# Optimization experiments

Hardware: AMD Instinct MI355X
Metric: run time of the kernel (lower is better)

## Reference

```python
import jax, jax.numpy as jnp
import numpy as np

# Model dims (match init_kwargs / input_specs)
B, L, D = 4, 1024, 512
CHI, S = 32, 4          # bond_dim, spatial_bond_dim
TRUNC_THR = 1e-4        # relative SVD truncation threshold
LN_EPS = 1e-6


def setup_inputs() -> dict:
    key = jax.random.key(0)
    ks = jax.random.split(key, 6)
    def dense(k, fi, fo):
        return jax.random.normal(k, (fi, fo), jnp.float32) / np.float32(np.sqrt(fi))
    return {
        "x": jax.random.normal(ks[0], (B, L, D), jnp.float32),
        "W_site": dense(ks[1], D, CHI * S * CHI),
        "b_site": jnp.zeros((CHI * S * CHI,), jnp.float32),
        "W_bridge": dense(ks[2], S * CHI, CHI),
        "b_bridge": jnp.zeros((CHI,), jnp.float32),
        "W_out": dense(ks[3], CHI, D),
        "b_out": jnp.zeros((D,), jnp.float32),
        "gamma": jnp.ones((D,), jnp.float32),
        "beta": jnp.zeros((D,), jnp.float32),
        "W_gate": dense(ks[4], D, D),
        "b_gate": jnp.zeros((D,), jnp.float32),
    }


def _mps_temporal_scan(x, site_weights):
    """Sequential O(L*chi^2) MPS scan with per-step SVD truncation.

    x: [B, L, D]; site_weights: [B, L, chi, s, chi].
    State h_t [B, chi] is the (normalized) left environment vector. Each step
    contracts the left vector (state + input injection from the first chi
    features, since initial_state is zeros) with the site tensor, truncates
    small singular values (relative threshold), and accumulates log-norms.
    Returns outputs [B, L, s*chi] and log_probs [B, L].
    """
    u_seq = jnp.transpose(x[:, :, :CHI], (1, 0, 2))            # [L, B, chi]
    A_seq = jnp.transpose(site_weights, (1, 0, 2, 3, 4))        # [L, B, chi, s, chi]

    def step(h, inp):
        A, u = inp                                              # [B,chi,s,chi], [B,chi]
        left = h + u                                            # input-driven left vector
        M = jnp.einsum('bl,blpr->bpr', left, A)                 # [B, s, chi]
        U, Sv, Vh = jnp.linalg.svd(M, full_matrices=False)      # Sv: [B, min(s,chi)]
        mask = (Sv >= TRUNC_THR * Sv[:, :1]).astype(M.dtype)    # relative truncation
        St = Sv * mask
        Mt = jnp.einsum('bik,bk,bkr->bir', U, St, Vh)           # truncated site matrix
        nrm = jnp.sqrt(jnp.sum(St * St, axis=-1) + 1e-12)       # Frobenius norm -> log prob
        v = jnp.sum(Mt, axis=1)                                 # contract physical index
        h_new = v / (jnp.linalg.norm(v, axis=-1, keepdims=True) + 1e-12)
        return h_new, (Mt.reshape(Mt.shape[0], -1), jnp.log(nrm))

    h0 = jnp.zeros((x.shape[0], CHI), x.dtype)                  # initial_state = zeros
    _, (outs, logp) = jax.lax.scan(step, h0, (A_seq, u_seq))
    return jnp.transpose(outs, (1, 0, 2)), jnp.transpose(logp, (1, 0))


def reference(x, W_site, b_site, W_bridge, b_bridge, W_out, b_out,
              gamma, beta, W_gate, b_gate):
    x = x.astype(jnp.float32)
    Bb, Ll = x.shape[0], x.shape[1]
    # site_tensor_proj: Dense(chi*s*chi) applied directly to inputs
    site_weights = (x @ W_site + b_site).reshape(Bb, Ll, CHI, S, CHI)
    outs, _logp = _mps_temporal_scan(x, site_weights)           # [B, L, s*chi]
    y = outs @ W_bridge + b_bridge                              # mps_bridge -> [B,L,chi]
    y = y @ W_out + b_out                                       # output_projection -> [B,L,D]
    # LayerNorm(eps=1e-6)
    mu = jnp.mean(y, axis=-1, keepdims=True)
    var = jnp.mean((y - mu) ** 2, axis=-1, keepdims=True)
    yn = (y - mu) * jax.lax.rsqrt(var + LN_EPS) * gamma + beta
    # gated residual
    gate = jax.nn.sigmoid(x @ W_gate + b_gate)
    return gate * yn + (1.0 - gate) * x
```

## Files before the change

kernel.cpp:

```cpp
#include <hip/hip_runtime.h>
#include <math.h>

#define B_   4
#define L_   1024
#define D_   512
#define CHI_ 32
#define S_   4
#define BT_  (B_ * L_)
#define NC_  2560
#define DPRE 8

__device__ __forceinline__ float readlane_f(float v, int l) {
    return __int_as_float(__builtin_amdgcn_readlane(__float_as_int(v), l));
}

__device__ __forceinline__ float bpermute_f(int byte_idx, float v) {
    return __int_as_float(__builtin_amdgcn_ds_bpermute(byte_idx, __float_as_int(v)));
}

template <int CTRL>
__device__ __forceinline__ float dpp_add(float x) {
    int y = __builtin_amdgcn_update_dpp(0, __float_as_int(x), CTRL, 0xf, 0xf, true);
    return x + __int_as_float(y);
}

__device__ __forceinline__ float reduce32_to_lane31(float x) {
    x = dpp_add<0x111>(x);
    x = dpp_add<0x112>(x);
    x = dpp_add<0x114>(x);
    x = dpp_add<0x118>(x);
    x = dpp_add<0x142>(x);
    return x;
}

__device__ __forceinline__ float octet_sum(float x) {
    x = dpp_add<0x111>(x);
    x = dpp_add<0x112>(x);
    x = dpp_add<0x114>(x);
    return x;
}

__global__ __launch_bounds__(256) void buildW_kernel(
    const float* __restrict__ Ws, const float* __restrict__ bs,
    const float* __restrict__ Wb, const float* __restrict__ Wg,
    const float* __restrict__ bg, float* __restrict__ Wcomb,
    float* __restrict__ biasC)
{
    const int tid = threadIdx.x;

    if (blockIdx.x == 512) {
        for (int f = tid; f < NC_; f += 256) {
            float acc;
            if (f < 1024) {
                const int q = f >> 8, rem = f & 255, i = rem >> 2, e = rem & 3;
                const int l = 4 * (i & 7) + e, r = (i >> 3) + 8 * q;
                const float* p = bs + l * 128 + r;
                acc = p[0] + p[32] + p[64] + p[96];
            } else if (f < 2048) {
                const int g = f - 1024, l = g >> 5, j = g & 31;
                acc = 0.f;
                for (int pr = 0; pr < 128; ++pr)
                    acc = fmaf(bs[l * 128 + pr], Wb[pr * 32 + j], acc);
            } else {
                acc = bg[f - 2048];
            }
            biasC[f] = acc;
        }
        return;
    }

    __shared__ float wsrow[4096];
    __shared__ float wbs[4096];

    const int d = blockIdx.x;
    #pragma unroll
    for (int i = 0; i < 16; ++i) {
        wsrow[i * 256 + tid] = Ws[(size_t)d * 4096 + i * 256 + tid];
        wbs[i * 256 + tid]   = Wb[i * 256 + tid];
    }
    __syncthreads();

    float* wrow = Wcomb + (size_t)d * NC_;

    #pragma unroll
    for (int ii = 0; ii < 4; ++ii) {
        const int f = ii * 256 + tid;
        const int q = f >> 8, rem = f & 255, i = rem >> 2, e = rem & 3;
        const int l = 4 * (i & 7) + e, r = (i >> 3) + 8 * q;
        const float* p = wsrow + l * 128 + r;
        wrow[f] = p[0] + p[32] + p[64] + p[96];
    }
    #pragma unroll
    for (int ii = 0; ii < 4; ++ii) {
        const int g = ii * 256 + tid;
        const int l = g >> 5, j = g & 31;
        float acc = 0.f;
        #pragma unroll 8
        for (int pr = 0; pr < 128; ++pr)
            acc = fmaf(wsrow[l * 128 + pr], wbs[pr * 32 + j], acc);
        wrow[1024 + g] = acc;
    }
    #pragma unroll
    for (int ii = 0; ii < 2; ++ii) {
        const int c = ii * 256 + tid;
        wrow[2048 + c] = Wg[(size_t)d * 512 + c];
    }
}

__global__ __launch_bounds__(256) void gemm_bias_kernel(
    const float* __restrict__ A, const float* __restrict__ Bm,
    const float* __restrict__ bias, float* __restrict__ C,
    int M, int N, int K)
{
    __shared__ float As[32][68];
    __shared__ float Bs[32][64];

    const int tid = threadIdx.x;
    const int tx = tid & 15;
    const int ty = tid >> 4;
    const int m0 = blockIdx.y * 64;
    const int n0 = blockIdx.x * 64;

    float c[4][4] = {};

    for (int k0 = 0; k0 < K; k0 += 32) {
        {
            const int o = tid * 8;
            const int m = o >> 5;
            const int k = o & 31;
            const float* ap = A + (size_t)(m0 + m) * K + k0 + k;
            const float4 a0 = *(const float4*)ap;
            const float4 a1 = *(const float4*)(ap + 4);
            As[k + 0][m] = a0.x; As[k + 1][m] = a0.y;
            As[k + 2][m] = a0.z; As[k + 3][m] = a0.w;
            As[k + 4][m] = a1.x; As[k + 5][m] = a1.y;
            As[k + 6][m] = a1.z; As[k + 7][m] = a1.w;
        }
        {
            const int o = tid * 8;
            const int k = o >> 6;
            const int n = o & 63;
            const float* bp = Bm + (size_t)(k0 + k) * N + n0 + n;
            *(float4*)&Bs[k][n]     = *(const float4*)bp;
            *(float4*)&Bs[k][n + 4] = *(const float4*)(bp + 4);
        }
        __syncthreads();

        #pragma unroll
        for (int kk = 0; kk < 32; ++kk) {
            const float4 av = *(const float4*)&As[kk][ty * 4];
            const float4 bv = *(const float4*)&Bs[kk][tx * 4];
            const float a[4] = {av.x, av.y, av.z, av.w};
            const float b[4] = {bv.x, bv.y, bv.z, bv.w};
            #pragma unroll
            for (int i = 0; i < 4; ++i)
                #pragma unroll
                for (int j = 0; j < 4; ++j)
                    c[i][j] = fmaf(a[i], b[j], c[i][j]);
        }
        __syncthreads();
    }

    const float4 bv = *(const float4*)&bias[n0 + tx * 4];
    #pragma unroll
    for (int i = 0; i < 4; ++i) {
        float4 outv;
        outv.x = c[i][0] + bv.x;
        outv.y = c[i][1] + bv.y;
        outv.z = c[i][2] + bv.z;
        outv.w = c[i][3] + bv.w;
        *(float4*)&C[(size_t)(m0 + ty * 4 + i) * N + n0 + tx * 4] = outv;
    }
}

__global__ __launch_bounds__(256) void cvec_kernel(
    const float* __restrict__ Cc, const float* __restrict__ x,
    float* __restrict__ cBuf)
{
    const int tid  = threadIdx.x;
    const int lane = tid & 63;
    const int bt   = blockIdx.x * 4 + (tid >> 6);

    const float* base = Cc + (size_t)bt * NC_ + 4 * lane;
    float4 a0 = *(const float4*)(base + 0);
    float4 a1 = *(const float4*)(base + 256);
    float4 a2 = *(const float4*)(base + 512);
    float4 a3 = *(const float4*)(base + 768);

    const float u = x[(size_t)bt * D_ + (lane & 31)];
    const int idx0 = 16 * (lane & 7);
    const float u0 = bpermute_f(idx0 + 0,  u);
    const float u1 = bpermute_f(idx0 + 4,  u);
    const float u2 = bpermute_f(idx0 + 8,  u);
    const float u3 = bpermute_f(idx0 + 12, u);

    float p0 = fmaf(u3, a0.w, fmaf(u2, a0.z, fmaf(u1, a0.y, u0 * a0.x)));
    float p1 = fmaf(u3, a1.w, fmaf(u2, a1.z, fmaf(u1, a1.y, u0 * a1.x)));
    float p2 = fmaf(u3, a2.w, fmaf(u2, a2.z, fmaf(u1, a2.y, u0 * a2.x)));
    float p3 = fmaf(u3, a3.w, fmaf(u2, a3.z, fmaf(u1, a3.y, u0 * a3.x)));

    p0 = octet_sum(p0); p1 = octet_sum(p1);
    p2 = octet_sum(p2); p3 = octet_sum(p3);

    if ((lane & 7) == 7) {
        const int k = lane >> 3;
        float* cp = cBuf + (size_t)bt * 32 + k;
        cp[0]  = p0;
        cp[8]  = p1;
        cp[16] = p2;
        cp[24] = p3;
    }
}

__global__ __launch_bounds__(64, 1) void scan_kernel(
    const float* __restrict__ Cc, const float* __restrict__ cBuf,
    float* __restrict__ wOut)
{
    const int b   = blockIdx.x;
    const int tid = threadIdx.x;

    const float* At = Cc + (size_t)b * L_ * NC_ + 4 * tid;
    const float* cb = cBuf + (size_t)b * L_ * 32 + (tid & 31);
    float*       wo = wOut + (size_t)b * L_ * 64 + tid;

    const int idx0 = 16 * (tid & 7);
    const int idxR = 32 * (tid & 7) + 28;
    const bool selA = (tid >> 3) & 1;
    const bool selB = (tid >> 4) & 1;

    float4 areg[DPRE][4];
    float  creg[DPRE];

    #pragma unroll
    for (int j = 0; j < DPRE; ++j) {
        const float* ap = At + (size_t)j * NC_;
        #pragma unroll
        for (int q = 0; q < 4; ++q) areg[j][q] = *(const float4*)(ap + 256 * q);
        creg[j] = cb[j * 32];
    }

    float w = 0.f;

    for (int t = 0; t < L_; t += DPRE) {
        #pragma unroll
        for (int j = 0; j < DPRE; ++j) {
            wo[(t + j) * 64] = w;

            float red = reduce32_to_lane31(w * w);

            const float wb0 = bpermute_f(idx0 + 0,  w);
            const float wb1 = bpermute_f(idx0 + 4,  w);
            const float wb2 = bpermute_f(idx0 + 8,  w);
            const float wb3 = bpermute_f(idx0 + 12, w);

            float p0, p1, p2, p3;
            {
                const float4 a0 = areg[j][0], a1 = areg[j][1];
                const float4 a2 = areg[j][2], a3 = areg[j][3];
                p0 = fmaf(wb3, a0.w, fmaf(wb2, a0.z, fmaf(wb1, a0.y, wb0 * a0.x)));
                p1 = fmaf(wb3, a1.w, fmaf(wb2, a1.z, fmaf(wb1, a1.y, wb0 * a1.x)));
                p2 = fmaf(wb3, a2.w, fmaf(wb2, a2.z, fmaf(wb1, a2.y, wb0 * a2.x)));
                p3 = fmaf(wb3, a3.w, fmaf(wb2, a3.z, fmaf(wb1, a3.y, wb0 * a3.x)));
            }

            p0 = octet_sum(p0);
            p1 = octet_sum(p1);
            p2 = octet_sum(p2);
            p3 = octet_sum(p3);

            const float m0 = bpermute_f(idxR, p0);
            const float m1 = bpermute_f(idxR, p1);
            const float m2 = bpermute_f(idxR, p2);
            const float m3 = bpermute_f(idxR, p3);
            const float t0 = selA ? m1 : m0;
            const float t1 = selA ? m3 : m2;
            const float m  = selB ? t1 : t0;

            const float n2 = readlane_f(red, 31);
            const float rn = rsqrtf(n2 + 1e-24f);
            w = fmaf(m, rn, creg[j]);

            int tn = t + j + DPRE;
            if (tn > L_ - 1) tn = L_ - 1;
            const float* ap = At + (size_t)tn * NC_;
            #pragma unroll
            for (int q = 0; q < 4; ++q) areg[j][q] = *(const float4*)(ap + 256 * q);
            creg[j] = cb[tn * 32];
        }
    }
}

__global__ __launch_bounds__(128) void phaseB_kernel(
    const float* __restrict__ Cc, const float* __restrict__ x,
    const float* __restrict__ wBuf, const float* __restrict__ bb,
    float* __restrict__ y1)
{
    __shared__ float lf[32];
    __shared__ float part[4][32];

    const int bt = blockIdx.x;
    const int tid = threadIdx.x;

    if (tid < 64) {
        const float wv = wBuf[(size_t)bt * 64 + tid];
        float red = reduce32_to_lane31(wv * wv);
        const float n2 = readlane_f(red, 31);
        const float rn = rsqrtf(n2 + 1e-24f);
        if (tid < 32)
            lf[tid] = fmaf(wv, rn, x[(size_t)bt * D_ + tid]);
    }
    __syncthreads();

    const int j = tid & 31, q = tid >> 5;
    const float* Gp = Cc + (size_t)bt * NC_ + 1024;
    float p = 0.f;
    #pragma unroll
    for (int i = 0; i < 8; ++i)
        p = fmaf(lf[8 * q + i], Gp[(8 * q + i) * 32 + j], p);
    part[q][j] = p;
    __syncthreads();

    if (tid < 32)
        y1[bt * 32 + tid] = part[0][tid] + part[1][tid] + part[2][tid]
                          + part[3][tid] + bb[tid];
}

__global__ __launch_bounds__(256) void epilogue_kernel(
    const float* __restrict__ x, const float* __restrict__ y1buf,
    const float* __restrict__ Wout, const float* __restrict__ bout,
    const float* __restrict__ gamma, const float* __restrict__ beta,
    const float* __restrict__ Cc, float* __restrict__ out)
{
    __shared__ float ys[32];
    __shared__ float red1[4], red2[4];

    const int bt = blockIdx.x;
    const int tid = threadIdx.x;

    if (tid < 32) ys[tid] = y1buf[bt * 32 + tid];
    __syncthreads();

    float yv[2];
    #pragma unroll
    for (int q = 0; q < 2; ++q) {
        const int d = tid + q * 256;
        float acc = bout[d];
        #pragma unroll
        for (int j = 0; j < 32; ++j)
            acc = fmaf(ys[j], Wout[j * D_ + d], acc);
        yv[q] = acc;
    }

    float s1 = yv[0] + yv[1];
    float s2 = yv[0] * yv[0] + yv[1] * yv[1];
    #pragma unroll
    for (int m = 1; m <= 32; m <<= 1) {
        s1 += __shfl_xor(s1, m);
        s2 += __shfl_xor(s2, m);
    }
    const int wid = tid >> 6;
    if ((tid & 63) == 0) { red1[wid] = s1; red2[wid] = s2; }
    __syncthreads();
    const float S1 = red1[0] + red1[1] + red1[2] + red1[3];
    const float S2 = red2[0] + red2[1] + red2[2] + red2[3];
    const float mu  = S1 * (1.f / (float)D_);
    const float var = S2 * (1.f / (float)D_) - mu * mu;
    const float rstd = rsqrtf(var + 1e-6f);

    #pragma unroll
    for (int q = 0; q < 2; ++q) {
        const int d = tid + q * 256;
        const size_t gi = (size_t)bt * D_ + d;
        const float yn = (yv[q] - mu) * rstd * gamma[d] + beta[d];
        const float z = Cc[(size_t)bt * NC_ + 2048 + d];
        const float g = 1.f / (1.f + expf(-z));
        const float xv = x[gi];
        out[gi] = g * yn + (1.f - g) * xv;
    }
}

extern "C" void kernel_launch(void* const* d_in, const int* in_sizes, int n_in,
                              void* d_out, int out_size, void* d_ws, size_t ws_size,
                              hipStream_t stream)
{
    const float* x        = (const float*)d_in[0];
    const float* W_site   = (const float*)d_in[1];
    const float* b_site   = (const float*)d_in[2];
    const float* W_bridge = (const float*)d_in[3];
    const float* b_bridge = (const float*)d_in[4];
    const float* W_out    = (const float*)d_in[5];
    const float* b_out    = (const float*)d_in[6];
    const float* gamma    = (const float*)d_in[7];
    const float* beta     = (const float*)d_in[8];
    const float* W_gate   = (const float*)d_in[9];
    const float* b_gate   = (const float*)d_in[10];
    float* out = (float*)d_out;

    float* ws = (float*)d_ws;
    float* Wcomb = ws;
    float* biasC = Wcomb + (size_t)512 * NC_;
    float* Cc    = biasC + NC_;
    float* cBuf  = Cc    + (size_t)BT_ * NC_;
    float* wBuf  = cBuf  + (size_t)BT_ * 32;
    float* y1    = wBuf  + (size_t)BT_ * 64;

    buildW_kernel<<<dim3(513), dim3(256), 0, stream>>>(
        W_site, b_site, W_bridge, W_gate, b_gate, Wcomb, biasC);

    gemm_bias_kernel<<<dim3(NC_ / 64, BT_ / 64), dim3(256), 0, stream>>>(
        x, Wcomb, biasC, Cc, BT_, NC_, D_);

    cvec_kernel<<<dim3(BT_ / 4), dim3(256), 0, stream>>>(Cc, x, cBuf);

    scan_kernel<<<dim3(B_), dim3(64), 0, stream>>>(Cc, cBuf, wBuf);

    phaseB_kernel<<<dim3(BT_), dim3(128), 0, stream>>>(
        Cc, x, wBuf, b_bridge, y1);

    epilogue_kernel<<<dim3(BT_), dim3(256), 0, stream>>>(
        x, y1, W_out, b_out, gamma, beta, Cc, out);
}
```

Measured before the change: 466.3 us.

## Stream scan site rows through LDS via async global_load_lds and fuse tail kernels

The sequential scan kernel now prefetches each upcoming timestep's site row and c-vector straight into an 8-slot LDS ring buffer with global_load_lds. Each step reads its operands back with hand-written ds_read and bpermute sequences that carry explicit waitcnt control. This replaces the deep register-resident prefetch and aims to cut register pressure and load latency on the latency-bound serial chain. Separately, the phaseB and epilogue kernels are merged into one tail kernel, removing a launch and the y1 round trip through global memory. The hand-tuned vmcnt(35) wait and the asm ordering are fragile and could give wrong results if the load counting is off.

```diff
diff --git a/kernel.cpp b/kernel.cpp
--- a/kernel.cpp
+++ b/kernel.cpp
@@ -8,7 +8,6 @@
 #define S_   4
 #define BT_  (B_ * L_)
 #define NC_  2560
-#define DPRE 8
 
 __device__ __forceinline__ float readlane_f(float v, int l) {
     return __int_as_float(__builtin_amdgcn_readlane(__float_as_int(v), l));
@@ -38,6 +37,22 @@
     x = dpp_add<0x112>(x);
     x = dpp_add<0x114>(x);
     return x;
+}
+
+__device__ __forceinline__ void dma16(const float* g, float* l) {
+    __builtin_amdgcn_global_load_lds(
+        (const __attribute__((address_space(1))) float*)g,
+        (__attribute__((address_space(3))) float*)l, 16, 0, 0);
+}
+__device__ __forceinline__ void dma4(const float* g, float* l) {
+    __builtin_amdgcn_global_load_lds(
+        (const __attribute__((address_space(1))) float*)g,
+        (__attribute__((address_space(3))) float*)l, 4, 0, 0);
+}
+
+__device__ __forceinline__ unsigned lds_off(const void* p) {
+    return (unsigned)(unsigned long long)
+        (const __attribute__((address_space(3))) void*)p;
 }
 
 __global__ __launch_bounds__(256) void buildW_kernel(
@@ -216,87 +231,125 @@
     const float* __restrict__ Cc, const float* __restrict__ cBuf,
     float* __restrict__ wOut)
 {
+    __shared__ __align__(16) float slots[8][1088];
+
     const int b   = blockIdx.x;
     const int tid = threadIdx.x;
 
-    const float* At = Cc + (size_t)b * L_ * NC_ + 4 * tid;
-    const float* cb = cBuf + (size_t)b * L_ * 32 + (tid & 31);
-    float*       wo = wOut + (size_t)b * L_ * 64 + tid;
-
-    const int idx0 = 16 * (tid & 7);
-    const int idxR = 32 * (tid & 7) + 28;
+    const float* Crow = Cc + (size_t)b * L_ * NC_;
+    const float* cb   = cBuf + (size_t)b * L_ * 32;
+    float*       wo   = wOut + (size_t)b * L_ * 64 + tid;
+
+    const int laneC = tid & 31;
+    const unsigned rowAddr = lds_off(&slots[0][0]) + 16u * (unsigned)tid;
+    const unsigned cAddr   = lds_off(&slots[0][0]) + 4096u + 4u * (unsigned)tid;
+
+    const int ia0 = 16 * (tid & 7) + 0;
+    const int ia1 = 16 * (tid & 7) + 4;
+    const int ia2 = 16 * (tid & 7) + 8;
+    const int ia3 = 16 * (tid & 7) + 12;
+    const int idxRv = 32 * (tid & 7) + 28;
     const bool selA = (tid >> 3) & 1;
     const bool selB = (tid >> 4) & 1;
 
-    float4 areg[DPRE][4];
-    float  creg[DPRE];
-
-    #pragma unroll
-    for (int j = 0; j < DPRE; ++j) {
-        const float* ap = At + (size_t)j * NC_;
+    #pragma unroll
+    for (int k = 0; k < 8; ++k) {
+        const float* rp = Crow + (size_t)k * NC_;
         #pragma unroll
-        for (int q = 0; q < 4; ++q) areg[j][q] = *(const float4*)(ap + 256 * q);
-        creg[j] = cb[j * 32];
+        for (int q = 0; q < 4; ++q)
+            dma16(rp + 256 * q + 4 * tid, &slots[k][256 * q]);
+        dma4(cb + k * 32 + laneC, &slots[k][1024]);
     }
 
     float w = 0.f;
 
-    for (int t = 0; t < L_; t += DPRE) {
+    for (int t = 0; t < L_; t += 8) {
         #pragma unroll
-        for (int j = 0; j < DPRE; ++j) {
-            wo[(t + j) * 64] = w;
+        for (int j = 0; j < 8; ++j) {
+            const int n = t + j;
 
             float red = reduce32_to_lane31(w * w);
 
-            const float wb0 = bpermute_f(idx0 + 0,  w);
-            const float wb1 = bpermute_f(idx0 + 4,  w);
-            const float wb2 = bpermute_f(idx0 + 8,  w);
-            const float wb3 = bpermute_f(idx0 + 12, w);
+            float wb0, wb1, wb2, wb3;
+            asm volatile(
+                "ds_bpermute_b32 %0, %4, %8\n\t"
+                "ds_bpermute_b32 %1, %5, %8\n\t"
+                "ds_bpermute_b32 %2, %6, %8\n\t"
+                "ds_bpermute_b32 %3, %7, %8"
+                : "=&v"(wb0), "=&v"(wb1), "=&v"(wb2), "=&v"(wb3)
+                : "v"(ia0), "v"(ia1), "v"(ia2), "v"(ia3), "v"(w));
+
+            float4 a0, a1, a2, a3;
+            float  cr;
+            {
+                const unsigned ra = rowAddr + (unsigned)(j * 4352);
+                const unsigned ca = cAddr   + (unsigned)(j * 4352);
+                asm volatile(
+                    "s_waitcnt vmcnt(35)\n\t"
+                    "ds_read_b128 %0, %5 offset:0\n\t"
+                    "ds_read_b128 %1, %5 offset:1024\n\t"
+                    "ds_read_b128 %2, %5 offset:2048\n\t"
+                    "ds_read_b128 %3, %5 offset:3072\n\t"
+                    "ds_read_b32  %4, %6\n\t"
+                    "s_waitcnt lgkmcnt(0)"
+                    : "=&v"(a0), "=&v"(a1), "=&v"(a2), "=&v"(a3), "=&v"(cr)
+                    : "v"(ra), "v"(ca));
+            }
+
+            wo[n * 64] = w;
+
+            {
+                int rowN = n + 8; if (rowN > L_ - 1) rowN = L_ - 1;
+                const float* rp = Crow + (size_t)rowN * NC_;
+                #pragma unroll
+                for (int q = 0; q < 4; ++q)
+                    dma16(rp + 256 * q + 4 * tid, &slots[j][256 * q]);
+                dma4(cb + rowN * 32 + laneC, &slots[j][1024]);
+            }
 
             float p0, p1, p2, p3;
-            {
-                const float4 a0 = areg[j][0], a1 = areg[j][1];
-                const float4 a2 = areg[j][2], a3 = areg[j][3];
-                p0 = fmaf(wb3, a0.w, fmaf(wb2, a0.z, fmaf(wb1, a0.y, wb0 * a0.x)));
-                p1 = fmaf(wb3, a1.w, fmaf(wb2, a1.z, fmaf(wb1, a1.y, wb0 * a1.x)));
-                p2 = fmaf(wb3, a2.w, fmaf(wb2, a2.z, fmaf(wb1, a2.y, wb0 * a2.x)));
-                p3 = fmaf(wb3, a3.w, fmaf(wb2, a3.z, fmaf(wb1, a3.y, wb0 * a3.x)));
-            }
+            p0 = fmaf(wb3, a0.w, fmaf(wb2, a0.z, fmaf(wb1, a0.y, wb0 * a0.x)));
+            p1 = fmaf(wb3, a1.w, fmaf(wb2, a1.z, fmaf(wb1, a1.y, wb0 * a1.x)));
+            p2 = fmaf(wb3, a2.w, fmaf(wb2, a2.z, fmaf(wb1, a2.y, wb0 * a2.x)));
+            p3 = fmaf(wb3, a3.w, fmaf(wb2, a3.z, fmaf(wb1, a3.y, wb0 * a3.x)));
 
             p0 = octet_sum(p0);
             p1 = octet_sum(p1);
             p2 = octet_sum(p2);
             p3 = octet_sum(p3);
 
-            const float m0 = bpermute_f(idxR, p0);
-            const float m1 = bpermute_f(idxR, p1);
-            const float m2 = bpermute_f(idxR, p2);
-            const float m3 = bpermute_f(idxR, p3);
+            float m0, m1, m2, m3;
+            asm volatile(
+                "ds_bpermute_b32 %0, %4, %5\n\t"
+                "ds_bpermute_b32 %1, %4, %6\n\t"
+                "ds_bpermute_b32 %2, %4, %7\n\t"
+                "ds_bpermute_b32 %3, %4, %8\n\t"
+                "s_waitcnt lgkmcnt(0)"
+                : "=&v"(m0), "=&v"(m1), "=&v"(m2), "=&v"(m3)
+                : "v"(idxRv), "v"(p0), "v"(p1), "v"(p2), "v"(p3));
+
             const float t0 = selA ? m1 : m0;
             const float t1 = selA ? m3 : m2;
             const float m  = selB ? t1 : t0;
 
-            const float n2 = readlane_f(red, 31);
-            const float rn = rsqrtf(n2 + 1e-24f);
-            w = fmaf(m, rn, creg[j]);
-
-            int tn = t + j + DPRE;
-            if (tn > L_ - 1) tn = L_ - 1;
-            const float* ap = At + (size_t)tn * NC_;
-            #pragma unroll
-            for (int q = 0; q < 4; ++q) areg[j][q] = *(const float4*)(ap + 256 * q);
-            creg[j] = cb[tn * 32];
+            const float n2   = readlane_f(red, 31);
+            const float rinv = rsqrtf(n2 + 1e-24f);
+            w = fmaf(m, rinv, cr);
         }
     }
 }
 
-__global__ __launch_bounds__(128) void phaseB_kernel(
+__global__ __launch_bounds__(256) void tail_kernel(
     const float* __restrict__ Cc, const float* __restrict__ x,
     const float* __restrict__ wBuf, const float* __restrict__ bb,
-    float* __restrict__ y1)
+    const float* __restrict__ Wout, const float* __restrict__ bout,
+    const float* __restrict__ gamma, const float* __restrict__ beta,
+    float* __restrict__ out)
 {
     __shared__ float lf[32];
     __shared__ float part[4][32];
+    __shared__ float ys[32];
+    __shared__ float red1[4], red2[4];
 
     const int bt = blockIdx.x;
     const int tid = threadIdx.x;
@@ -311,33 +364,19 @@
     }
     __syncthreads();
 
-    const int j = tid & 31, q = tid >> 5;
-    const float* Gp = Cc + (size_t)bt * NC_ + 1024;
-    float p = 0.f;
-    #pragma unroll
-    for (int i = 0; i < 8; ++i)
-        p = fmaf(lf[8 * q + i], Gp[(8 * q + i) * 32 + j], p);
-    part[q][j] = p;
+    if (tid < 128) {
+        const int j = tid & 31, q = tid >> 5;
+        const float* Gp = Cc + (size_t)bt * NC_ + 1024;
+        float p = 0.f;
+        #pragma unroll
+        for (int i = 0; i < 8; ++i)
+            p = fmaf(lf[8 * q + i], Gp[(8 * q + i) * 32 + j], p);
+        part[q][j] = p;
+    }
     __syncthreads();
-
     if (tid < 32)
-        y1[bt * 32 + tid] = part[0][tid] + part[1][tid] + part[2][tid]
-                          + part[3][tid] + bb[tid];
-}
-
-__global__ __launch_bounds__(256) void epilogue_kernel(
-    const float* __restrict__ x, const float* __restrict__ y1buf,
-    const float* __restrict__ Wout, const float* __restrict__ bout,
-    const float* __restrict__ gamma, const float* __restrict__ beta,
-    const float* __restrict__ Cc, float* __restrict__ out)
-{
-    __shared__ float ys[32];
-    __shared__ float red1[4], red2[4];
-
-    const int bt = blockIdx.x;
-    const int tid = threadIdx.x;
-
-    if (tid < 32) ys[tid] = y1buf[bt * 32 + tid];
+        ys[tid] = part[0][tid] + part[1][tid] + part[2][tid] + part[3][tid]
+                + bb[tid];
     __syncthreads();
 
     float yv[2];
@@ -402,7 +441,6 @@
     float* Cc    = biasC + NC_;
     float* cBuf  = Cc    + (size_t)BT_ * NC_;
     float* wBuf  = cBuf  + (size_t)BT_ * 32;
-    float* y1    = wBuf  + (size_t)BT_ * 64;
 
     buildW_kernel<<<dim3(513), dim3(256), 0, stream>>>(
         W_site, b_site, W_bridge, W_gate, b_gate, Wcomb, biasC);
@@ -414,9 +452,6 @@
 
     scan_kernel<<<dim3(B_), dim3(64), 0, stream>>>(Cc, cBuf, wBuf);
 
-    phaseB_kernel<<<dim3(BT_), dim3(128), 0, stream>>>(
-        Cc, x, wBuf, b_bridge, y1);
-
-    epilogue_kernel<<<dim3(BT_), dim3(256), 0, stream>>>(
-        x, y1, W_out, b_out, gamma, beta, Cc, out);
-}
+    tail_kernel<<<dim3(BT_), dim3(256), 0, stream>>>(
+        Cc, x, wBuf, b_bridge, W_out, b_out, gamma, beta, out);
+}
```

Result: slower. 502.7 us (+7.8%).
